# Kernel tuning notes

Measured on AMD Instinct MI355X. Metric: run time of the kernel, lower is better.

Reference implementation:

```python
import jax, jax.numpy as jnp
import numpy as np

# Module config (matches init_kwargs)
T, B, C = 2048, 8, 1024   # seq_len, batch, input_size
H, K = 16, 31             # num_heads, kernel_size
PAD_L = 30                # padding_l (causal)


def setup_inputs() -> dict:
    key = jax.random.key(0)
    k1, k2 = jax.random.split(key)
    x = jax.random.normal(k1, (T, B, C), dtype=jnp.float32)
    # nn.Parameter(num_heads, kernel_size), xavier-init approximated by randn
    weight = jax.random.normal(k2, (H, K), dtype=jnp.float32)
    return {"x": x, "weight": weight}


def reference(x, weight):
    # x: (T, B, C); weight: (H, K)
    # weight_softmax=True: softmax over kernel taps per head
    w = jax.nn.softmax(weight, axis=-1)  # (H, K)
    # permute to (B, C, T) as the CUDA kernel expects
    x_bct = jnp.transpose(x, (1, 2, 0))
    # expand per-head kernel to per-channel depthwise kernel: (C, 1, K)
    w_ck = jnp.repeat(w, C // H, axis=0)[:, None, :]
    # lightconv: out[b,c,t] = sum_k w[head(c),k] * x_pad[b,c,t+k],
    # left pad = PAD_L, right pad = K-1-PAD_L (causal when PAD_L=K-1).
    # conv_general_dilated is cross-correlation, matching the CUDA kernel.
    out = jax.lax.conv_general_dilated(
        x_bct, w_ck,
        window_strides=(1,),
        padding=[(PAD_L, K - 1 - PAD_L)],
        dimension_numbers=("NCH", "OIH", "NCH"),
        feature_group_count=C,
    )  # (B, C, T)
    # bias=False, so just permute back to (T, B, C)
    return jnp.transpose(out, (2, 0, 1))
```

## Files before the change

### kernel.cpp

```cpp
#include <hip/hip_runtime.h>
#include <math.h>

#define T_LEN 2048
#define B_SZ  8
#define C_SZ  1024
#define NH    16
#define KW    31
#define HALO  (KW - 1)
#define TT    8
#define CHUNK 64
#define NTILE (CHUNK / TT)
#define RING  32
#define WIN   (TT + HALO)
#define CGW   128
#define ROWSTRIDE (B_SZ * C_SZ)

#define GLOBAL_AS(p) ((const __attribute__((address_space(1))) void*)(p))
#define LDS_AS(p)    ((__attribute__((address_space(3))) void*)(p))

__global__ __launch_bounds__(64, 3) void lightconv_kernel(
    const float* __restrict__ x, const float* __restrict__ weight,
    float* __restrict__ out) {
  __shared__ float ring[RING][CGW];
  const int lane = threadIdx.x;

  const int cgrp = blockIdx.x & 7;
  const int tc   = blockIdx.x >> 3;
  const int b    = blockIdx.y;
  const int c0   = cgrp * CGW;
  const int tb   = tc * CHUNK;

  const int head = cgrp * 2 + (lane >> 5);
  float wv[KW];
  float m = -1e30f;
#pragma unroll
  for (int k = 0; k < KW; ++k) {
    wv[k] = weight[head * KW + k];
    m = fmaxf(m, wv[k]);
  }
  float s = 0.f;
#pragma unroll
  for (int k = 0; k < KW; ++k) {
    wv[k] = expf(wv[k] - m);
    s += wv[k];
  }
  const float inv = 1.f / s;
  float wk[KW];
#pragma unroll
  for (int k = 0; k < KW; ++k) wk[k] = wv[k] * inv;

  const float* xbase = x + (size_t)b * C_SZ + c0;
  const float* xch   = xbase + 2 * lane;
  const int lane_off = (lane >> 5) * ROWSTRIDE + (lane & 31) * 4;

  float2 xv[WIN];
  if (tb == 0) {
#pragma unroll
    for (int i = 0; i < HALO; ++i) xv[i] = make_float2(0.f, 0.f);
  } else {
#pragma unroll
    for (int i = 0; i < HALO; ++i) {
      xv[i] = *(const float2*)&xch[(size_t)(tb - HALO + i) * ROWSTRIDE];
    }
  }
#pragma unroll
  for (int r2 = 0; r2 < 8; ++r2) {
    const float* gp = xbase + (size_t)(tb + 2 * r2) * ROWSTRIDE + lane_off;
    __builtin_amdgcn_global_load_lds(GLOBAL_AS(gp), LDS_AS(&ring[2 * r2][0]),
                                     16, 0, 0);
  }

#pragma unroll
  for (int j = 0; j < NTILE; ++j) {
    const int tstart = tb + j * TT;

    if (j <= NTILE - 3) {
#pragma unroll
      for (int r2 = 0; r2 < 4; ++r2) {
        const float* gp =
            xbase + (size_t)(tstart + 2 * TT + 2 * r2) * ROWSTRIDE + lane_off;
        __builtin_amdgcn_global_load_lds(
            GLOBAL_AS(gp), LDS_AS(&ring[(8 * j + 16 + 2 * r2) & (RING - 1)][0]),
            16, 0, 0);
      }
    }
    if (j == 0)                asm volatile("s_waitcnt vmcnt(8)"  ::: "memory");
    else if (j == 1)           asm volatile("s_waitcnt vmcnt(16)" ::: "memory");
    else if (j == NTILE - 2)   asm volatile("s_waitcnt vmcnt(20)" ::: "memory");
    else if (j == NTILE - 1)   asm volatile("s_waitcnt vmcnt(16)" ::: "memory");
    else                       asm volatile("s_waitcnt vmcnt(24)" ::: "memory");
    __builtin_amdgcn_sched_barrier(0);

#pragma unroll
    for (int i = 0; i < TT; ++i) {
      const float2* rp = (const float2*)&ring[(8 * j + i) & (RING - 1)][0];
      xv[HALO + i] = rp[lane];
    }
    float* opb = out + ((size_t)tstart * B_SZ + b) * C_SZ + c0 + 2 * lane;
#pragma unroll
    for (int o = 0; o < TT; ++o) {
      float ax = 0.f, ay = 0.f;
#pragma unroll
      for (int k = 0; k < KW; ++k) {
        ax = fmaf(wk[k], xv[o + k].x, ax);
        ay = fmaf(wk[k], xv[o + k].y, ay);
      }
      *(float2*)&opb[(size_t)o * ROWSTRIDE] = make_float2(ax, ay);
    }
#pragma unroll
    for (int i = 0; i < HALO; ++i) xv[i] = xv[i + TT];
  }
}

extern "C" void kernel_launch(void* const* d_in, const int* in_sizes, int n_in,
                              void* d_out, int out_size, void* d_ws, size_t ws_size,
                              hipStream_t stream) {
  const float* x = (const float*)d_in[0];
  const float* w = (const float*)d_in[1];
  float* out = (float*)d_out;
  (void)in_sizes; (void)n_in; (void)out_size; (void)d_ws; (void)ws_size;

  dim3 grid((C_SZ / CGW) * (T_LEN / CHUNK), B_SZ);
  dim3 block(64);
  lightconv_kernel<<<grid, block, 0, stream>>>(x, w, out);
}
```

Baseline: 30.27 us.

## Split block into one producer wave and two compute waves sharing the LDS ring

The block grows from one wave to three. Wave 0 only issues the asynchronous global-to-LDS loads into the ring buffer and waits on vmcnt. It then signals each tile with a workgroup barrier. The other two waves each handle one head's 64 channels, one scalar channel per lane, and read their tile from LDS after the barrier. Softmax weights are made wave-uniform with readfirstlane so they can live in scalar registers. This is meant to separate memory latency from FMA work and cut per-lane register pressure, at the cost of a barrier on every tile and an idle producer wave.

```diff
diff --git a/kernel.cpp b/kernel.cpp
--- a/kernel.cpp
+++ b/kernel.cpp
@@ -18,11 +18,13 @@
 #define GLOBAL_AS(p) ((const __attribute__((address_space(1))) void*)(p))
 #define LDS_AS(p)    ((__attribute__((address_space(3))) void*)(p))
 
-__global__ __launch_bounds__(64, 3) void lightconv_kernel(
+__global__ __launch_bounds__(192, 4) void lightconv_kernel(
     const float* __restrict__ x, const float* __restrict__ weight,
     float* __restrict__ out) {
   __shared__ float ring[RING][CGW];
-  const int lane = threadIdx.x;
+  const int tid  = threadIdx.x;
+  const int w    = tid >> 6;
+  const int lane = tid & 63;
 
   const int cgrp = blockIdx.x & 7;
   const int tc   = blockIdx.x >> 3;
@@ -30,85 +32,91 @@
   const int c0   = cgrp * CGW;
   const int tb   = tc * CHUNK;
 
-  const int head = cgrp * 2 + (lane >> 5);
-  float wv[KW];
-  float m = -1e30f;
+  const float* xbase = x + (size_t)b * C_SZ + c0;
+
+  if (w == 0) {
+    const int lane_off = (lane >> 5) * ROWSTRIDE + (lane & 31) * 4;
 #pragma unroll
-  for (int k = 0; k < KW; ++k) {
-    wv[k] = weight[head * KW + k];
-    m = fmaxf(m, wv[k]);
-  }
-  float s = 0.f;
+    for (int r2 = 0; r2 < 8; ++r2) {
+      const float* gp = xbase + (size_t)(tb + 2 * r2) * ROWSTRIDE + lane_off;
+      __builtin_amdgcn_global_load_lds(GLOBAL_AS(gp), LDS_AS(&ring[2 * r2][0]),
+                                       16, 0, 0);
+    }
 #pragma unroll
-  for (int k = 0; k < KW; ++k) {
-    wv[k] = expf(wv[k] - m);
-    s += wv[k];
-  }
-  const float inv = 1.f / s;
-  float wk[KW];
+    for (int j = 0; j < NTILE; ++j) {
+      __builtin_amdgcn_sched_barrier(0);
+      if (j <= NTILE - 3) {
 #pragma unroll
-  for (int k = 0; k < KW; ++k) wk[k] = wv[k] * inv;
+        for (int r2 = 0; r2 < 4; ++r2) {
+          const float* gp =
+              xbase + (size_t)(tb + (j + 2) * TT + 2 * r2) * ROWSTRIDE + lane_off;
+          __builtin_amdgcn_global_load_lds(
+              GLOBAL_AS(gp), LDS_AS(&ring[(8 * j + 16 + 2 * r2) & (RING - 1)][0]),
+              16, 0, 0);
+        }
+      }
+      if (j <= NTILE - 3)      asm volatile("s_waitcnt vmcnt(8)" ::: "memory");
+      else if (j == NTILE - 2) asm volatile("s_waitcnt vmcnt(4)" ::: "memory");
+      else                     asm volatile("s_waitcnt vmcnt(0)" ::: "memory");
+      __builtin_amdgcn_sched_barrier(0);
+      __builtin_amdgcn_s_barrier();
+    }
+  } else {
+    const int choff = (w - 1) * 64;
+    const int head  = cgrp * 2 + (w - 1);
 
-  const float* xbase = x + (size_t)b * C_SZ + c0;
-  const float* xch   = xbase + 2 * lane;
-  const int lane_off = (lane >> 5) * ROWSTRIDE + (lane & 31) * 4;
+    float wv[KW];
+    float m = -1e30f;
+#pragma unroll
+    for (int k = 0; k < KW; ++k) {
+      wv[k] = weight[head * KW + k];
+      m = fmaxf(m, wv[k]);
+    }
+    float s = 0.f;
+#pragma unroll
+    for (int k = 0; k < KW; ++k) {
+      wv[k] = expf(wv[k] - m);
+      s += wv[k];
+    }
+    const float inv = 1.f / s;
+    float wk[KW];
+#pragma unroll
+    for (int k = 0; k < KW; ++k) {
+      wk[k] = __uint_as_float(
+          __builtin_amdgcn_readfirstlane(__float_as_uint(wv[k] * inv)));
+    }
 
-  float2 xv[WIN];
-  if (tb == 0) {
+    const float* xch = xbase + choff + lane;
+    float xv[WIN];
+    if (tb == 0) {
 #pragma unroll
-    for (int i = 0; i < HALO; ++i) xv[i] = make_float2(0.f, 0.f);
-  } else {
+      for (int i = 0; i < HALO; ++i) xv[i] = 0.f;
+    } else {
 #pragma unroll
-    for (int i = 0; i < HALO; ++i) {
-      xv[i] = *(const float2*)&xch[(size_t)(tb - HALO + i) * ROWSTRIDE];
-    }
-  }
-#pragma unroll
-  for (int r2 = 0; r2 < 8; ++r2) {
-    const float* gp = xbase + (size_t)(tb + 2 * r2) * ROWSTRIDE + lane_off;
-    __builtin_amdgcn_global_load_lds(GLOBAL_AS(gp), LDS_AS(&ring[2 * r2][0]),
-                                     16, 0, 0);
-  }
-
-#pragma unroll
-  for (int j = 0; j < NTILE; ++j) {
-    const int tstart = tb + j * TT;
-
-    if (j <= NTILE - 3) {
-#pragma unroll
-      for (int r2 = 0; r2 < 4; ++r2) {
-        const float* gp =
-            xbase + (size_t)(tstart + 2 * TT + 2 * r2) * ROWSTRIDE + lane_off;
-        __builtin_amdgcn_global_load_lds(
-            GLOBAL_AS(gp), LDS_AS(&ring[(8 * j + 16 + 2 * r2) & (RING - 1)][0]),
-            16, 0, 0);
+      for (int i = 0; i < HALO; ++i) {
+        xv[i] = xch[(size_t)(tb - HALO + i) * ROWSTRIDE];
       }
     }
-    if (j == 0)                asm volatile("s_waitcnt vmcnt(8)"  ::: "memory");
-    else if (j == 1)           asm volatile("s_waitcnt vmcnt(16)" ::: "memory");
-    else if (j == NTILE - 2)   asm volatile("s_waitcnt vmcnt(20)" ::: "memory");
-    else if (j == NTILE - 1)   asm volatile("s_waitcnt vmcnt(16)" ::: "memory");
-    else                       asm volatile("s_waitcnt vmcnt(24)" ::: "memory");
-    __builtin_amdgcn_sched_barrier(0);
 
+    float* opb = out + ((size_t)tb * B_SZ + b) * C_SZ + c0 + choff + lane;
 #pragma unroll
-    for (int i = 0; i < TT; ++i) {
-      const float2* rp = (const float2*)&ring[(8 * j + i) & (RING - 1)][0];
-      xv[HALO + i] = rp[lane];
+    for (int j = 0; j < NTILE; ++j) {
+      __builtin_amdgcn_s_barrier();
+      __builtin_amdgcn_sched_barrier(0);
+#pragma unroll
+      for (int i = 0; i < TT; ++i) {
+        xv[HALO + i] = ring[(8 * j + i) & (RING - 1)][choff + lane];
+      }
+#pragma unroll
+      for (int o = 0; o < TT; ++o) {
+        float a = 0.f;
+#pragma unroll
+        for (int k = 0; k < KW; ++k) a = fmaf(wk[k], xv[o + k], a);
+        opb[(size_t)(j * TT + o) * ROWSTRIDE] = a;
+      }
+#pragma unroll
+      for (int i = 0; i < HALO; ++i) xv[i] = xv[i + TT];
     }
-    float* opb = out + ((size_t)tstart * B_SZ + b) * C_SZ + c0 + 2 * lane;
-#pragma unroll
-    for (int o = 0; o < TT; ++o) {
-      float ax = 0.f, ay = 0.f;
-#pragma unroll
-      for (int k = 0; k < KW; ++k) {
-        ax = fmaf(wk[k], xv[o + k].x, ax);
-        ay = fmaf(wk[k], xv[o + k].y, ay);
-      }
-      *(float2*)&opb[(size_t)o * ROWSTRIDE] = make_float2(ax, ay);
-    }
-#pragma unroll
-    for (int i = 0; i < HALO; ++i) xv[i] = xv[i + TT];
   }
 }
 
@@ -121,6 +129,6 @@
   (void)in_sizes; (void)n_in; (void)out_size; (void)d_ws; (void)ws_size;
 
   dim3 grid((C_SZ / CGW) * (T_LEN / CHUNK), B_SZ);
-  dim3 block(64);
+  dim3 block(192);
   lightconv_kernel<<<grid, block, 0, stream>>>(x, w, out);
 }
```

After: 37.26 us. 1.23x slower.

## Widen per-thread work to four channels and remap block tile order

Applied to the files above, without the earlier changes.

Each lane now processes four adjacent channels with float4 loads and stores instead of two. The channel group grows to 256, which halves the number of blocks, and the async global-to-LDS prefetch issues one full row per load with rescaled vmcnt waits. Block indices are also remapped so neighbouring blocks walk time chunks within a channel group. The aim is fewer, wider memory transactions and amortized per-block setup such as the softmax and halo load. The cost is much higher register pressure (a 38-entry float4 window), which forces occupancy down to two waves, and fewer blocks to hide latency.

```diff
diff --git a/kernel.cpp b/kernel.cpp
--- a/kernel.cpp
+++ b/kernel.cpp
@@ -12,25 +12,27 @@
 #define NTILE (CHUNK / TT)
 #define RING  32
 #define WIN   (TT + HALO)
-#define CGW   128
+#define CGW   256
 #define ROWSTRIDE (B_SZ * C_SZ)
 
 #define GLOBAL_AS(p) ((const __attribute__((address_space(1))) void*)(p))
 #define LDS_AS(p)    ((__attribute__((address_space(3))) void*)(p))
 
-__global__ __launch_bounds__(64, 3) void lightconv_kernel(
+__global__ __launch_bounds__(64, 2) void lightconv_kernel(
     const float* __restrict__ x, const float* __restrict__ weight,
     float* __restrict__ out) {
   __shared__ float ring[RING][CGW];
   const int lane = threadIdx.x;
 
-  const int cgrp = blockIdx.x & 7;
-  const int tc   = blockIdx.x >> 3;
+  const int bx   = blockIdx.x;
+  const int lin  = (bx & 7) * 16 + (bx >> 3);
+  const int tc   = lin & 31;
+  const int cgrp = lin >> 5;
   const int b    = blockIdx.y;
   const int c0   = cgrp * CGW;
   const int tb   = tc * CHUNK;
 
-  const int head = cgrp * 2 + (lane >> 5);
+  const int head = cgrp * 4 + (lane >> 4);
   float wv[KW];
   float m = -1e30f;
 #pragma unroll
@@ -50,23 +52,25 @@
   for (int k = 0; k < KW; ++k) wk[k] = wv[k] * inv;
 
   const float* xbase = x + (size_t)b * C_SZ + c0;
-  const float* xch   = xbase + 2 * lane;
-  const int lane_off = (lane >> 5) * ROWSTRIDE + (lane & 31) * 4;
+  const float* xch   = xbase + 4 * lane;
+  const int lane_off = lane * 4;
 
-  float2 xv[WIN];
+  float4 xv[WIN];
   if (tb == 0) {
 #pragma unroll
-    for (int i = 0; i < HALO; ++i) xv[i] = make_float2(0.f, 0.f);
+    for (int i = 0; i < HALO; ++i) xv[i] = make_float4(0.f, 0.f, 0.f, 0.f);
   } else {
 #pragma unroll
     for (int i = 0; i < HALO; ++i) {
-      xv[i] = *(const float2*)&xch[(size_t)(tb - HALO + i) * ROWSTRIDE];
+      xv[i] = *(const float4*)&xch[(size_t)(tb - HALO + i) * ROWSTRIDE];
     }
   }
+  __builtin_amdgcn_sched_barrier(0);
+
 #pragma unroll
-  for (int r2 = 0; r2 < 8; ++r2) {
-    const float* gp = xbase + (size_t)(tb + 2 * r2) * ROWSTRIDE + lane_off;
-    __builtin_amdgcn_global_load_lds(GLOBAL_AS(gp), LDS_AS(&ring[2 * r2][0]),
+  for (int r = 0; r < 16; ++r) {
+    const float* gp = xbase + (size_t)(tb + r) * ROWSTRIDE + lane_off;
+    __builtin_amdgcn_global_load_lds(GLOBAL_AS(gp), LDS_AS(&ring[r][0]),
                                      16, 0, 0);
   }
 
@@ -74,38 +78,42 @@
   for (int j = 0; j < NTILE; ++j) {
     const int tstart = tb + j * TT;
 
+    __builtin_amdgcn_sched_barrier(0);
     if (j <= NTILE - 3) {
 #pragma unroll
-      for (int r2 = 0; r2 < 4; ++r2) {
+      for (int r = 0; r < TT; ++r) {
         const float* gp =
-            xbase + (size_t)(tstart + 2 * TT + 2 * r2) * ROWSTRIDE + lane_off;
+            xbase + (size_t)(tstart + 2 * TT + r) * ROWSTRIDE + lane_off;
         __builtin_amdgcn_global_load_lds(
-            GLOBAL_AS(gp), LDS_AS(&ring[(8 * j + 16 + 2 * r2) & (RING - 1)][0]),
+            GLOBAL_AS(gp), LDS_AS(&ring[(8 * j + 16 + r) & (RING - 1)][0]),
             16, 0, 0);
       }
     }
-    if (j == 0)                asm volatile("s_waitcnt vmcnt(8)"  ::: "memory");
-    else if (j == 1)           asm volatile("s_waitcnt vmcnt(16)" ::: "memory");
-    else if (j == NTILE - 2)   asm volatile("s_waitcnt vmcnt(20)" ::: "memory");
+    if (j == 0)                asm volatile("s_waitcnt vmcnt(16)" ::: "memory");
+    else if (j == 1)           asm volatile("s_waitcnt vmcnt(24)" ::: "memory");
+    else if (j == NTILE - 2)   asm volatile("s_waitcnt vmcnt(24)" ::: "memory");
     else if (j == NTILE - 1)   asm volatile("s_waitcnt vmcnt(16)" ::: "memory");
-    else                       asm volatile("s_waitcnt vmcnt(24)" ::: "memory");
+    else                       asm volatile("s_waitcnt vmcnt(32)" ::: "memory");
     __builtin_amdgcn_sched_barrier(0);
 
 #pragma unroll
     for (int i = 0; i < TT; ++i) {
-      const float2* rp = (const float2*)&ring[(8 * j + i) & (RING - 1)][0];
+      const float4* rp = (const float4*)&ring[(8 * j + i) & (RING - 1)][0];
       xv[HALO + i] = rp[lane];
     }
-    float* opb = out + ((size_t)tstart * B_SZ + b) * C_SZ + c0 + 2 * lane;
+    float* opb = out + ((size_t)tstart * B_SZ + b) * C_SZ + c0 + 4 * lane;
 #pragma unroll
     for (int o = 0; o < TT; ++o) {
-      float ax = 0.f, ay = 0.f;
+      float ax = 0.f, ay = 0.f, az = 0.f, aw = 0.f;
 #pragma unroll
       for (int k = 0; k < KW; ++k) {
-        ax = fmaf(wk[k], xv[o + k].x, ax);
-        ay = fmaf(wk[k], xv[o + k].y, ay);
+        const float w = wk[k];
+        ax = fmaf(w, xv[o + k].x, ax);
+        ay = fmaf(w, xv[o + k].y, ay);
+        az = fmaf(w, xv[o + k].z, az);
+        aw = fmaf(w, xv[o + k].w, aw);
       }
-      *(float2*)&opb[(size_t)o * ROWSTRIDE] = make_float2(ax, ay);
+      *(float4*)&opb[(size_t)o * ROWSTRIDE] = make_float4(ax, ay, az, aw);
     }
 #pragma unroll
     for (int i = 0; i < HALO; ++i) xv[i] = xv[i + TT];
```

Result: slower. 32.31 us (+6.7%).
